# Kernel optimization log

Measured on AMD Instinct MI355X. Metric: run time of the kernel, lower is better.

The kernel has to match this reference:

```python
import jax, jax.numpy as jnp
import numpy as np

L, H, D, DFF, B, S = 4, 8, 512, 2048, 2, 2048
DH = D // H
EPS = 1e-5
SCALE_BASE = 512.0


def setup_inputs() -> dict:
    key = jax.random.key(0)
    ks = jax.random.split(key, 8)
    def w(k, shape, s=0.02):
        return jax.random.normal(k, shape, jnp.float32) * s
    return {
        "x": jax.random.normal(ks[0], (B, S, D), jnp.float32),
        "WQ": w(ks[1], (L, H, D, DH)),
        "WK": w(ks[2], (L, H, D, DH)),
        "WV": w(ks[3], (L, H, D, DH)),
        "WG": w(ks[4], (L, D, D)),
        "WO": w(ks[5], (L, D, D)),
        "gn_w": jnp.ones((L, D), jnp.float32),
        "gn_b": jnp.zeros((L, D), jnp.float32),
        "ln1_w": jnp.ones((L, D), jnp.float32),
        "ln1_b": jnp.zeros((L, D), jnp.float32),
        "ln2_w": jnp.ones((L, D), jnp.float32),
        "ln2_b": jnp.zeros((L, D), jnp.float32),
        "ffn_w1": w(ks[6], (L, D, DFF)),
        "ffn_b1": jnp.zeros((L, DFF), jnp.float32),
        "ffn_w2": w(ks[7], (L, DFF, D)),
        "ffn_b2": jnp.zeros((L, D), jnp.float32),
    }


def _dup(t):
    # duplicate_interleave: [a,b] -> [a,a,b,b]
    return jnp.repeat(t, 2, axis=-1)


def _rot(x):
    # rotate_every_two: (x1,x2) -> (-x2, x1)
    x1, x2 = x[..., ::2], x[..., 1::2]
    return jnp.stack([-x2, x1], axis=-1).reshape(x.shape)


def _xpos(x, downscale):
    # x: [B,H,S,dh]  XPOS rotary with length-extrapolating scale
    s_len, dh = x.shape[-2], x.shape[-1]
    half = dh // 2
    base = (jnp.arange(0, dh, 2, dtype=jnp.float32) + 0.4 * dh) / (1.4 * dh)  # [half]
    power = jnp.arange(s_len, dtype=jnp.float32) / SCALE_BASE
    scale = base[None, :] ** power[:, None]  # [S, half]
    if downscale:
        scale = 1.0 / scale
    inv_freq = 1.0 / (10000.0 ** (jnp.arange(half, dtype=jnp.float32) / half))
    ang = jnp.arange(s_len, dtype=jnp.float32)[:, None] * inv_freq[None, :]
    sin, cos, sc = _dup(jnp.sin(ang)), _dup(jnp.cos(ang)), _dup(scale)
    return x * cos * sc + _rot(x) * sin * sc


def _ln(x, w, b):
    mu = jnp.mean(x, -1, keepdims=True)
    var = jnp.mean((x - mu) ** 2, -1, keepdims=True)
    return (x - mu) * jax.lax.rsqrt(var + EPS) * w + b


def reference(x, WQ, WK, WV, WG, WO, gn_w, gn_b, ln1_w, ln1_b, ln2_w, ln2_b, ffn_w1, ffn_b1, ffn_w2, ffn_b2):
    gammas = 1.0 - jnp.exp(jnp.linspace(np.log(1.0 / 32.0), np.log(1.0 / 512.0), H)).astype(jnp.float32)
    idx = jnp.arange(S, dtype=jnp.float32)
    diff = idx[:, None] - idx[None, :]
    Dmask = jnp.where(diff >= 0, gammas[:, None, None] ** diff, 0.0)  # [H,S,S]
    b = x.shape[0]
    for i in range(L):
        xn = _ln(x, ln1_w[i], ln1_b[i])
        q = _xpos(jnp.einsum('bsd,hde->bhse', xn, WQ[i]), False)
        k = _xpos(jnp.einsum('bsd,hde->bhse', xn, WK[i]), True)
        v = jnp.einsum('bsd,hde->bhse', xn, WV[i])
        att = jnp.einsum('bhse,bhte->bhst', q, k) * Dmask[None]  # [B,H,S,S]
        yh = jnp.einsum('bhst,bhte->bhse', att, v)               # [B,H,S,dh]
        yh = yh.transpose(0, 2, 1, 3)                            # [B,S,H,dh]
        mu = jnp.mean(yh, -1, keepdims=True)
        var = jnp.mean((yh - mu) ** 2, -1, keepdims=True)
        yn = (yh - mu) * jax.lax.rsqrt(var + EPS)
        yn = yn * gn_w[i].reshape(H, DH) + gn_b[i].reshape(H, DH)
        y = yn.reshape(b, S, D)
        g = jax.nn.silu(xn @ WG[i])
        y1 = (g * y) @ WO[i] + x
        h = _ln(y1, ln2_w[i], ln2_b[i])
        x = jax.nn.gelu(h @ ffn_w1[i] + ffn_b1[i], approximate=False) @ ffn_w2[i] + ffn_b2[i] + y1
    return x
```

## Files before the change

### kernel.cpp

```cpp
#include <hip/hip_runtime.h>
#include <hip/hip_bf16.h>

#define LYR 4
#define NH  8
#define DM  512
#define DHD 64
#define DFF 2048
#define BB  2
#define SSL 2048
#define NROWS (BB*SSL)

typedef unsigned short u16;
typedef __attribute__((ext_vector_type(8))) short bf16x8;
typedef __attribute__((ext_vector_type(4))) float f32x4;
typedef __attribute__((ext_vector_type(4))) unsigned int u32x4;

__device__ __forceinline__ u16 f2bf(float f) {
    union { float f; unsigned u; } v; v.f = f;
    unsigned r = v.u + 0x7FFFu + ((v.u >> 16) & 1u);
    return (u16)(r >> 16);
}
__device__ __forceinline__ float bf2f(u16 b) {
    union { unsigned u; float f; } v; v.u = ((unsigned)b) << 16;
    return v.f;
}
__device__ __forceinline__ int swz(int row, int col) {
    return row * 64 + (col & 7) + ((((col >> 3) ^ row) & 7) << 3);
}
__device__ __forceinline__ int swzP(int row, int col) {
    return row * 128 + (col & 7) + ((((col >> 3) ^ row) & 15) << 3);
}
__device__ __forceinline__ void gload16(const u16* g, u16* l) {
    __builtin_amdgcn_global_load_lds(
        (const __attribute__((address_space(1))) unsigned int*)g,
        (__attribute__((address_space(3))) unsigned int*)l, 16, 0, 0);
}
template <int N> __device__ __forceinline__ void wait_vmcnt() {
    if constexpr (N == 0)      asm volatile("s_waitcnt vmcnt(0)" ::: "memory");
    else if constexpr (N == 6) asm volatile("s_waitcnt vmcnt(6)" ::: "memory");
    else if constexpr (N == 8) asm volatile("s_waitcnt vmcnt(8)" ::: "memory");
    else static_assert(N == 0 || N == 6 || N == 8, "unsupported vmcnt");
}
__device__ __forceinline__ void block_barrier() {
    __builtin_amdgcn_s_barrier();
    asm volatile("" ::: "memory");
}


__global__ __launch_bounds__(256) void xpos_tables(float4* __restrict__ tab4) {
    const int idx = blockIdx.x * 256 + threadIdx.x;
    const int s = idx >> 5, j = idx & 31;
    const float base = (2.f * j + 0.4f * 64.f) / (1.4f * 64.f);
    const float invf = powf(10000.f, -(float)j / 32.f);
    const float ang = (float)s * invf;
    const float scq = powf(base, (float)s / 512.f);
    tab4[idx] = make_float4(sinf(ang), cosf(ang), scq, 1.f / scq);
}

__global__ __launch_bounds__(256)
void prep_qkv(const float* __restrict__ WQp, const float* __restrict__ WKp,
              const float* __restrict__ WVp, u16* __restrict__ WBT) {
    const int dt = blockIdx.x;
    const int h = blockIdx.y & 7, which = blockIdx.y >> 3;
    const int l = blockIdx.z;
    const float* W = (which == 0 ? WQp : which == 1 ? WKp : WVp);
    const float* ip = W + ((size_t)(l * 8 + h)) * (512 * 64);
    u16* op = WBT + (size_t)l * (2048 * 512) + (size_t)(which * 512 + h * 64) * 512;
    __shared__ u16 tile[64 * 72];
    const int t = threadIdx.x, rr = t >> 2, cc = (t & 3) * 16;
    const float* src = ip + (size_t)(dt * 64 + rr) * 64 + cc;
#pragma unroll
    for (int i = 0; i < 16; ++i) tile[rr * 72 + cc + i] = f2bf(src[i]);
    __syncthreads();
    u16 tmp[16] __attribute__((aligned(16)));
#pragma unroll
    for (int i = 0; i < 16; ++i) tmp[i] = tile[(cc + i) * 72 + rr];
    u16* dst = op + (size_t)rr * 512 + dt * 64 + cc;
    *(u32x4*)&dst[0] = *(const u32x4*)&tmp[0];
    *(u32x4*)&dst[8] = *(const u32x4*)&tmp[8];
}

__global__ __launch_bounds__(256)
void prep_t(const float* __restrict__ in, u16* __restrict__ out, int R, int C,
            long long in_ls, long long out_ls) {
    const float* ip = in + (size_t)blockIdx.z * in_ls;
    u16* op = out + (size_t)blockIdx.z * out_ls;
    const int r0 = blockIdx.x * 64, c0t = blockIdx.y * 64;
    __shared__ u16 tile[64 * 72];
    const int t = threadIdx.x, rr = t >> 2, cc = (t & 3) * 16;
    const float* src = ip + (size_t)(r0 + rr) * C + c0t + cc;
#pragma unroll
    for (int i = 0; i < 16; ++i) tile[rr * 72 + cc + i] = f2bf(src[i]);
    __syncthreads();
    u16 tmp[16] __attribute__((aligned(16)));
#pragma unroll
    for (int i = 0; i < 16; ++i) tmp[i] = tile[(cc + i) * 72 + rr];
    u16* dst = op + (size_t)(c0t + rr) * R + r0 + cc;
    *(u32x4*)&dst[0] = *(const u32x4*)&tmp[0];
    *(u32x4*)&dst[8] = *(const u32x4*)&tmp[8];
}

__global__ __launch_bounds__(256)
void ln_kernel(const float* __restrict__ x, const float* __restrict__ wt,
               const float* __restrict__ bs, u16* __restrict__ out) {
    const int row = blockIdx.x * 4 + (threadIdx.x >> 6);
    const int lane = threadIdx.x & 63;
    const float* xr = x + (size_t)row * DM + lane * 8;
    float v[8];
    *(float4*)&v[0] = *(const float4*)&xr[0];
    *(float4*)&v[4] = *(const float4*)&xr[4];
    float s = 0.f, s2 = 0.f;
#pragma unroll
    for (int i = 0; i < 8; ++i) { s += v[i]; s2 += v[i] * v[i]; }
#pragma unroll
    for (int m = 1; m < 64; m <<= 1) {
        s  += __shfl_xor(s, m, 64);
        s2 += __shfl_xor(s2, m, 64);
    }
    const float mu = s * (1.f / DM);
    const float rs = rsqrtf(s2 * (1.f / DM) - mu * mu + 1e-5f);
    const int e0 = lane * 8;
    u16 o[8] __attribute__((aligned(16)));
#pragma unroll
    for (int i = 0; i < 8; ++i)
        o[i] = f2bf((v[i] - mu) * rs * wt[e0 + i] + bs[e0 + i]);
    *(u32x4*)&out[(size_t)row * DM + e0] = *(const u32x4*)o;
}

template <int BM, int BN, int EPI>
__global__ __launch_bounds__(256)
void gemm_bt(const u16* __restrict__ A, const u16* __restrict__ Bt,
             u16* __restrict__ obf, float* __restrict__ of32,
             const float* __restrict__ res, const float* __restrict__ bias,
             u16* __restrict__ qb, u16* __restrict__ kb, u16* __restrict__ vt,
             u16* __restrict__ gb, const float4* __restrict__ tab4,
             int M, int N, int K) {
    constexpr int FM = BM / 32, FN = BN / 32;
    constexpr int LPS = BM / 32 + BN / 32;
    static_assert(LPS == 6, "vmcnt template expects 6");
    __shared__ __align__(16) u16 As[2][BM * 64];
    __shared__ __align__(16) u16 Bs[2][BN * 64];
    const int t = threadIdx.x;
    const int lane = t & 63, w4 = t >> 6;
    const int wr = w4 >> 1, wc = w4 & 1;
    const int fr = lane & 15, fq = lane >> 4;
    const int nX = N / BN;
    const int nwg = (M / BM) * nX;
    const int swzid = (blockIdx.x & 7) * (nwg >> 3) + (blockIdx.x >> 3);
    const int m0 = (swzid / nX) * BM, n0 = (swzid % nX) * BN;
    const int lr = lane >> 3;
    const int ls = lane & 7;
    const int nsteps = K >> 6;

    auto stage = [&](int step, int slot) {
        const int k0 = step << 6;
#pragma unroll
        for (int q = 0; q < BM / 32; ++q) {
            const int ib = q * 4 + w4;
            const int row = ib * 8 + lr;
            const int cc = ls ^ (row & 7);
            gload16(&A[(size_t)(m0 + row) * K + k0 + cc * 8], &As[slot][ib * 512]);
        }
#pragma unroll
        for (int q = 0; q < BN / 32; ++q) {
            const int ib = q * 4 + w4;
            const int row = ib * 8 + lr;
            const int cc = ls ^ (row & 7);
            gload16(&Bt[(size_t)(n0 + row) * K + k0 + cc * 8], &Bs[slot][ib * 512]);
        }
    };

    f32x4 acc[FM][FN] = {};
    stage(0, 0);
    stage(1, 1);
    for (int st = 0; st < nsteps; ++st) {
        if (st + 1 < nsteps) wait_vmcnt<LPS>(); else wait_vmcnt<0>();
        __builtin_amdgcn_sched_barrier(0);
        block_barrier();
        const u16* Ac = As[st & 1];
        const u16* Bc = Bs[st & 1];
#pragma unroll
        for (int ks = 0; ks < 2; ++ks) {
            bf16x8 av[FM], bv[FN];
#pragma unroll
            for (int i = 0; i < FM; ++i)
                av[i] = *(const bf16x8*)&Ac[swz(wr * (BM / 2) + i * 16 + fr, ks * 32 + fq * 8)];
#pragma unroll
            for (int j = 0; j < FN; ++j)
                bv[j] = *(const bf16x8*)&Bc[swz(wc * (BN / 2) + j * 16 + fr, ks * 32 + fq * 8)];
#pragma unroll
            for (int i = 0; i < FM; ++i)
#pragma unroll
                for (int j = 0; j < FN; ++j)
                    acc[i][j] = __builtin_amdgcn_mfma_f32_16x16x32_bf16(av[i], bv[j], acc[i][j], 0, 0, 0);
        }
        asm volatile("s_waitcnt lgkmcnt(0)" ::: "memory");
        __builtin_amdgcn_sched_barrier(0);
        block_barrier();
        if (st + 2 < nsteps) stage(st + 2, st & 1);
    }

    if constexpr (EPI == 4) {
        const int region = n0 >> 9;
        const int h = (n0 & 511) >> 6;
        const int b = m0 >> 11;
        const int bh = b * NH + h;
        const int s0 = m0 & 2047;
        if (region == 3) {
#pragma unroll
            for (int i = 0; i < FM; ++i)
#pragma unroll
                for (int j = 0; j < FN; ++j)
#pragma unroll
                    for (int r = 0; r < 4; ++r) {
                        const int m = m0 + wr * (BM / 2) + i * 16 + fq * 4 + r;
                        const int e = wc * (BN / 2) + j * 16 + fr;
                        gb[(size_t)m * 512 + h * 64 + e] = f2bf(acc[i][j][r]);
                    }
        } else if (region <= 1) {
            u16* dst = (region == 0) ? qb : kb;
#pragma unroll
            for (int i = 0; i < FM; ++i)
#pragma unroll
                for (int j = 0; j < FN; ++j)
#pragma unroll
                    for (int r = 0; r < 4; ++r) {
                        const int s = s0 + wr * (BM / 2) + i * 16 + fq * 4 + r;
                        const int e = wc * (BN / 2) + j * 16 + fr;
                        const float v = acc[i][j][r];
                        const float p = __shfl_xor(v, 1, 64);
                        const float rot = (e & 1) ? p : -p;
                        const float4 t4 = tab4[(size_t)s * 32 + (e >> 1)];
                        const float scl = (region == 0) ? t4.z : t4.w;
                        dst[((size_t)bh * 2048 + s) * 64 + e] =
                            f2bf((v * t4.y + rot * t4.x) * scl);
                    }
        } else {
            constexpr int LTS = BM + 8;
            u16* LT = (u16*)As;
#pragma unroll
            for (int i = 0; i < FM; ++i)
#pragma unroll
                for (int j = 0; j < FN; ++j)
#pragma unroll
                    for (int r = 0; r < 4; ++r) {
                        const int sl = wr * (BM / 2) + i * 16 + fq * 4 + r;
                        const int e = wc * (BN / 2) + j * 16 + fr;
                        LT[e * LTS + sl] = f2bf(acc[i][j][r]);
                    }
            __syncthreads();
            for (int c = t; c < 64 * (BM / 8); c += 256) {
                const int er = c / (BM / 8);
                const int sc = (c % (BM / 8)) * 8;
                const u32x4 vrow = *(const u32x4*)&LT[er * LTS + sc];
                *(u32x4*)&vt[((size_t)bh * 64 + er) * 2048 + s0 + sc] = vrow;
            }
        }
    } else {
#pragma unroll
        for (int i = 0; i < FM; ++i)
#pragma unroll
            for (int j = 0; j < FN; ++j)
#pragma unroll
                for (int r = 0; r < 4; ++r) {
                    const int m = m0 + wr * (BM / 2) + i * 16 + fq * 4 + r;
                    const int n = n0 + wc * (BN / 2) + j * 16 + fr;
                    const size_t idx = (size_t)m * N + n;
                    float v = acc[i][j][r];
                    if constexpr (EPI == 0) {
                        obf[idx] = f2bf(v);
                    } else if constexpr (EPI == 1) {
                        of32[idx] = v + res[idx];
                    } else if constexpr (EPI == 2) {
                        float tt = v + bias[n];
                        obf[idx] = f2bf(0.5f * tt * (1.f + erff(tt * 0.7071067811865475f)));
                    } else {
                        of32[idx] = v + bias[n] + res[idx];
                    }
                }
    }
}

__global__ __launch_bounds__(512)
void retention(const u16* __restrict__ Qb, const u16* __restrict__ Kb,
               const u16* __restrict__ Vt, const u16* __restrict__ gate,
               const float* __restrict__ gnw, const float* __restrict__ gnb,
               u16* __restrict__ zb) {
    extern __shared__ __align__(16) char smem[];
    u16* KsB = (u16*)smem;
    u16* VsB = (u16*)(smem + 32768);
    u16* Qs  = (u16*)(smem + 65536);
    u16* Ps  = (u16*)(smem + 73728);

    const int logical = (blockIdx.x & 7) * 64 + (blockIdx.x >> 3);
    const int bh = logical >> 5;
    const int qt = 31 - (logical & 31);
    const int h = bh & 7, b = bh >> 3;
    const int t = threadIdx.x;
    const int lane = t & 63, w = t >> 6;
    const int fr = lane & 15, fq = lane >> 4;
    const int wr = w & 1, wc2 = w >> 1;
    const int oc = wc2 & 1, th = w >> 2;

    const float gamma = 1.f - expf(-3.4657359f + (float)h * -0.39608410f);
    const float lgam = log2f(gamma);
    const float dlim = 19.931568f / (-lgam);
    const int jt_last = (qt * 64 + 63) >> 7;
    int jt_min = 0;
    {
        const float need = (float)(qt * 64 - 127) - dlim;
        if (need > 0.f) jt_min = (int)ceilf(need * (1.f / 128.f));
        if (jt_min > jt_last) jt_min = jt_last;
        if (jt_min < 0) jt_min = 0;
    }

    float rowf[2][4], colf[2];
#pragma unroll
    for (int i = 0; i < 2; ++i)
#pragma unroll
        for (int rr = 0; rr < 4; ++rr)
            rowf[i][rr] = exp2f((float)(wr * 32 + i * 16 + fq * 4 + rr) * lgam);
#pragma unroll
    for (int j = 0; j < 2; ++j)
        colf[j] = exp2f(-(float)(wc2 * 32 + j * 16 + fr) * lgam);

    const size_t bh2048 = (size_t)bh * 2048;
    const int lr8 = lane >> 3, ls8 = lane & 7;
    const int lr16 = lane >> 4, ls16 = lane & 15;

    {
        const int row = w * 8 + lr8;
        const int cc = ls8 ^ (row & 7);
        gload16(&Qb[(bh2048 + qt * 64 + row) * 64 + cc * 8], &Qs[w * 512]);
    }

    f32x4 oacc[2][2] = {};
    int cur = 0;
    {
        const int jt = jt_min;
        u16* Kd = KsB; u16* Vd = VsB;
#pragma unroll
        for (int q = 0; q < 2; ++q) {
            const int row = q * 64 + w * 8 + lr8;
            const int cc = ls8 ^ (row & 7);
            gload16(&Kb[(bh2048 + jt * 128 + row) * 64 + cc * 8], &Kd[(q * 64 + w * 8) * 64]);
        }
#pragma unroll
        for (int q = 0; q < 2; ++q) {
            const int row = w * 8 + q * 4 + lr16;
            const int cc = ls16 ^ (row & 15);
            gload16(&Vt[((size_t)bh * 64 + row) * 2048 + jt * 128 + cc * 8], &Vd[(w * 8 + q * 4) * 128]);
        }
    }

    for (int jt = jt_min; jt <= jt_last; ++jt) {
        __syncthreads();
        if (jt < jt_last) {
            const int nb = cur ^ 1;
            u16* Kd = KsB + nb * 8192;
            u16* Vd = VsB + nb * 8192;
#pragma unroll
            for (int q = 0; q < 2; ++q) {
                const int row = q * 64 + w * 8 + lr8;
                const int cc = ls8 ^ (row & 7);
                gload16(&Kb[(bh2048 + (jt + 1) * 128 + row) * 64 + cc * 8], &Kd[(q * 64 + w * 8) * 64]);
            }
#pragma unroll
            for (int q = 0; q < 2; ++q) {
                const int row = w * 8 + q * 4 + lr16;
                const int cc = ls16 ^ (row & 15);
                gload16(&Vt[((size_t)bh * 64 + row) * 2048 + (jt + 1) * 128 + cc * 8], &Vd[(w * 8 + q * 4) * 128]);
            }
        }
        const u16* Kc = KsB + cur * 8192;
        f32x4 sac[2][2] = {};
#pragma unroll
        for (int ks = 0; ks < 2; ++ks) {
            bf16x8 qa[2], kb2[2];
#pragma unroll
            for (int i = 0; i < 2; ++i)
                qa[i] = *(const bf16x8*)&Qs[swz(wr * 32 + i * 16 + fr, ks * 32 + fq * 8)];
#pragma unroll
            for (int j = 0; j < 2; ++j)
                kb2[j] = *(const bf16x8*)&Kc[swz(wc2 * 32 + j * 16 + fr, ks * 32 + fq * 8)];
#pragma unroll
            for (int i = 0; i < 2; ++i)
#pragma unroll
                for (int j = 0; j < 2; ++j)
                    sac[i][j] = __builtin_amdgcn_mfma_f32_16x16x32_bf16(qa[i], kb2[j], sac[i][j], 0, 0, 0);
        }
        const float sc = exp2f((float)(qt * 64 - jt * 128) * lgam);
        const bool diag = (jt == jt_last);
#pragma unroll
        for (int i = 0; i < 2; ++i)
#pragma unroll
            for (int j = 0; j < 2; ++j)
#pragma unroll
                for (int rr = 0; rr < 4; ++rr) {
                    float m = sc * rowf[i][rr] * colf[j];
                    if (diag) {
                        const int d = (qt * 64 + wr * 32 + i * 16 + fq * 4 + rr)
                                    - (jt * 128 + wc2 * 32 + j * 16 + fr);
                        if (d < 0) m = 0.f;
                    }
                    Ps[swzP(wr * 32 + i * 16 + fq * 4 + rr, wc2 * 32 + j * 16 + fr)] =
                        f2bf(sac[i][j][rr] * m);
                }
        __syncthreads();
        const u16* Vc = VsB + cur * 8192;
#pragma unroll
        for (int ks = 0; ks < 2; ++ks) {
            const int tcol = th * 64 + ks * 32 + fq * 8;
            bf16x8 pa[2], vb[2];
#pragma unroll
            for (int i = 0; i < 2; ++i)
                pa[i] = *(const bf16x8*)&Ps[swzP(wr * 32 + i * 16 + fr, tcol)];
#pragma unroll
            for (int j = 0; j < 2; ++j)
                vb[j] = *(const bf16x8*)&Vc[swzP(oc * 32 + j * 16 + fr, tcol)];
#pragma unroll
            for (int i = 0; i < 2; ++i)
#pragma unroll
                for (int j = 0; j < 2; ++j)
                    oacc[i][j] = __builtin_amdgcn_mfma_f32_16x16x32_bf16(pa[i], vb[j], oacc[i][j], 0, 0, 0);
        }
        cur ^= 1;
    }

    __syncthreads();
    float* Of = (float*)smem;
    if (th == 1) {
#pragma unroll
        for (int i = 0; i < 2; ++i)
#pragma unroll
            for (int j = 0; j < 2; ++j)
#pragma unroll
                for (int rr = 0; rr < 4; ++rr)
                    Of[(wr * 32 + i * 16 + fq * 4 + rr) * 66 + oc * 32 + j * 16 + fr] = oacc[i][j][rr];
    }
    __syncthreads();
    if (th == 0) {
#pragma unroll
        for (int i = 0; i < 2; ++i)
#pragma unroll
            for (int j = 0; j < 2; ++j)
#pragma unroll
                for (int rr = 0; rr < 4; ++rr) {
                    const int idx = (wr * 32 + i * 16 + fq * 4 + rr) * 66 + oc * 32 + j * 16 + fr;
                    Of[idx] += oacc[i][j][rr];
                }
    }
    __syncthreads();
    const int row = t >> 3, c0 = (t & 7) * 8;
    float v[8];
    float s = 0.f, s2 = 0.f;
#pragma unroll
    for (int i = 0; i < 8; ++i) {
        v[i] = Of[row * 66 + c0 + i];
        s += v[i]; s2 += v[i] * v[i];
    }
    s  += __shfl_xor(s, 1, 64);  s  += __shfl_xor(s, 2, 64);  s  += __shfl_xor(s, 4, 64);
    s2 += __shfl_xor(s2, 1, 64); s2 += __shfl_xor(s2, 2, 64); s2 += __shfl_xor(s2, 4, 64);
    const float mu = s * (1.f / 64.f);
    const float rs = rsqrtf(s2 * (1.f / 64.f) - mu * mu + 1e-5f);
    const int sg = qt * 64 + row;
    u16 gv[8] __attribute__((aligned(16)));
    *(u32x4*)gv = *(const u32x4*)&gate[((size_t)(b * SSL + sg)) * 512 + h * 64 + c0];
    u16 ob[8] __attribute__((aligned(16)));
#pragma unroll
    for (int i = 0; i < 8; ++i) {
        const int dc = h * 64 + c0 + i;
        const float yn = (v[i] - mu) * rs * gnw[dc] + gnb[dc];
        const float g = bf2f(gv[i]);
        ob[i] = f2bf(yn * (g / (1.f + expf(-g))));
    }
    *(u32x4*)&zb[((size_t)(b * SSL + sg)) * 512 + h * 64 + c0] = *(const u32x4*)ob;
}

extern "C" void kernel_launch(void* const* d_in, const int* in_sizes, int n_in,
                              void* d_out, int out_size, void* d_ws, size_t ws_size,
                              hipStream_t stream) {
    const float* X    = (const float*)d_in[0];
    const float* WQ   = (const float*)d_in[1];
    const float* WK   = (const float*)d_in[2];
    const float* WV   = (const float*)d_in[3];
    const float* WG   = (const float*)d_in[4];
    const float* WO   = (const float*)d_in[5];
    const float* GNW  = (const float*)d_in[6];
    const float* GNB  = (const float*)d_in[7];
    const float* LN1W = (const float*)d_in[8];
    const float* LN1B = (const float*)d_in[9];
    const float* LN2W = (const float*)d_in[10];
    const float* LN2B = (const float*)d_in[11];
    const float* FW1  = (const float*)d_in[12];
    const float* FB1  = (const float*)d_in[13];
    const float* FW2  = (const float*)d_in[14];
    const float* FB2  = (const float*)d_in[15];

    char* ws = (char*)d_ws;
    size_t off = 0;
    auto alloc = [&](size_t n) { char* p = ws + off; off += (n + 255) & ~(size_t)255; return p; };

    u16*   WBT  = (u16*)alloc((size_t)LYR * 2048 * 512 * 2);
    u16*   WOT  = (u16*)alloc((size_t)LYR * 512 * 512 * 2);
    u16*   W1T  = (u16*)alloc((size_t)LYR * 2048 * 512 * 2);
    u16*   W2T  = (u16*)alloc((size_t)LYR * 512 * 2048 * 2);
    float4* TAB4 = (float4*)alloc((size_t)2048 * 32 * 16);
    float* XB   = (float*)alloc((size_t)NROWS * DM * 4);
    u16*   XN   = (u16*)alloc((size_t)NROWS * DM * 2);
    u16*   FF1  = (u16*)alloc((size_t)NROWS * 2048 * 2);
    u16*   GB   = (u16*)alloc((size_t)NROWS * DM * 2);
    u16*   QBp  = (u16*)alloc((size_t)NROWS * DM * 2);
    u16*   KBp  = (u16*)alloc((size_t)NROWS * DM * 2);
    u16*   VTp  = (u16*)alloc((size_t)NROWS * DM * 2);
    u16*   ZB   = (u16*)alloc((size_t)NROWS * DM * 2);
    float* Y1   = (float*)alloc((size_t)NROWS * DM * 4);
    u16*   HB   = QBp;

    xpos_tables<<<256, 256, 0, stream>>>(TAB4);
    prep_qkv<<<dim3(8, 24, LYR), 256, 0, stream>>>(WQ, WK, WV, WBT);
    prep_t<<<dim3(8, 8, LYR), 256, 0, stream>>>(WG, WBT + 1536 * 512, 512, 512,
                                                (long long)512 * 512, (long long)2048 * 512);
    prep_t<<<dim3(8, 8, LYR), 256, 0, stream>>>(WO, WOT, 512, 512,
                                                (long long)512 * 512, (long long)512 * 512);
    prep_t<<<dim3(8, 32, LYR), 256, 0, stream>>>(FW1, W1T, 512, 2048,
                                                 (long long)512 * 2048, (long long)2048 * 512);
    prep_t<<<dim3(32, 8, LYR), 256, 0, stream>>>(FW2, W2T, 2048, 512,
                                                 (long long)2048 * 512, (long long)512 * 2048);

    for (int l = 0; l < LYR; ++l) {
        const float* xsrc = (l == 0) ? X : XB;
        float* xdst = (l == LYR - 1) ? (float*)d_out : XB;
        ln_kernel<<<NROWS / 4, 256, 0, stream>>>(xsrc, LN1W + l * 512, LN1B + l * 512, XN);
        gemm_bt<128, 64, 4><<<1024, 256, 0, stream>>>(
            XN, WBT + (size_t)l * 2048 * 512, nullptr, nullptr, nullptr, nullptr,
            QBp, KBp, VTp, GB, TAB4, NROWS, 2048, 512);
        retention<<<512, 512, 90112, stream>>>(QBp, KBp, VTp, GB,
                                               GNW + l * 512, GNB + l * 512, ZB);
        gemm_bt<64, 128, 1><<<256, 256, 0, stream>>>(
            ZB, WOT + (size_t)l * 512 * 512, nullptr, Y1, xsrc, nullptr,
            nullptr, nullptr, nullptr, nullptr, nullptr, NROWS, 512, 512);
        ln_kernel<<<NROWS / 4, 256, 0, stream>>>(Y1, LN2W + l * 512, LN2B + l * 512, HB);
        gemm_bt<128, 64, 2><<<1024, 256, 0, stream>>>(
            HB, W1T + (size_t)l * 2048 * 512, FF1, nullptr, nullptr, FB1 + l * 2048,
            nullptr, nullptr, nullptr, nullptr, nullptr, NROWS, 2048, 512);
        gemm_bt<64, 128, 3><<<256, 256, 0, stream>>>(
            FF1, W2T + (size_t)l * 512 * 2048, nullptr, xdst, Y1, FB2 + l * 512,
            nullptr, nullptr, nullptr, nullptr, nullptr, NROWS, 512, 2048);
    }
}
```

Before: 477.3 us.

## Add 256x128 tiled 512-thread GEMM for QKV/gate and FFN1 projections

Adds a new gemm_big kernel with 256x128 tiles, 8 waves per block and launch_bounds(512,1). It replaces the 128x64 gemm_bt for the QKV+gate projection and the FFN up-projection with GELU. The larger tiles raise operand reuse from LDS and cut the block count from 1024 to 256, and s_setprio is raised around the MFMA loop. The XPOS and V-transpose epilogues are adapted so one tile can span two heads. In exchange there are fewer blocks to spread across CUs (256) and more register pressure from 16 accumulators per wave.

```diff
diff --git a/kernel.cpp b/kernel.cpp
--- a/kernel.cpp
+++ b/kernel.cpp
@@ -38,8 +38,7 @@
 template <int N> __device__ __forceinline__ void wait_vmcnt() {
     if constexpr (N == 0)      asm volatile("s_waitcnt vmcnt(0)" ::: "memory");
     else if constexpr (N == 6) asm volatile("s_waitcnt vmcnt(6)" ::: "memory");
-    else if constexpr (N == 8) asm volatile("s_waitcnt vmcnt(8)" ::: "memory");
-    else static_assert(N == 0 || N == 6 || N == 8, "unsupported vmcnt");
+    else static_assert(N == 0 || N == 6, "unsupported vmcnt");
 }
 __device__ __forceinline__ void block_barrier() {
     __builtin_amdgcn_s_barrier();
@@ -132,8 +131,6 @@
 void gemm_bt(const u16* __restrict__ A, const u16* __restrict__ Bt,
              u16* __restrict__ obf, float* __restrict__ of32,
              const float* __restrict__ res, const float* __restrict__ bias,
-             u16* __restrict__ qb, u16* __restrict__ kb, u16* __restrict__ vt,
-             u16* __restrict__ gb, const float4* __restrict__ tab4,
              int M, int N, int K) {
     constexpr int FM = BM / 32, FN = BN / 32;
     constexpr int LPS = BM / 32 + BN / 32;
@@ -199,85 +196,161 @@
         block_barrier();
         if (st + 2 < nsteps) stage(st + 2, st & 1);
     }
-
-    if constexpr (EPI == 4) {
+#pragma unroll
+    for (int i = 0; i < FM; ++i)
+#pragma unroll
+        for (int j = 0; j < FN; ++j)
+#pragma unroll
+            for (int r = 0; r < 4; ++r) {
+                const int m = m0 + wr * (BM / 2) + i * 16 + fq * 4 + r;
+                const int n = n0 + wc * (BN / 2) + j * 16 + fr;
+                const size_t idx = (size_t)m * N + n;
+                float v = acc[i][j][r];
+                if constexpr (EPI == 1) {
+                    of32[idx] = v + res[idx];
+                } else {
+                    of32[idx] = v + bias[n] + res[idx];
+                }
+            }
+}
+
+template <int EPI>
+__global__ __launch_bounds__(512, 1)
+void gemm_big(const u16* __restrict__ A, const u16* __restrict__ Bt,
+              u16* __restrict__ obf, const float* __restrict__ bias,
+              u16* __restrict__ qb, u16* __restrict__ kb, u16* __restrict__ vt,
+              u16* __restrict__ gb, const float4* __restrict__ tab4,
+              int M, int N, int K) {
+    constexpr int BM = 256, BN = 128;
+    __shared__ __align__(16) u16 SM[49152];
+    const int t = threadIdx.x;
+    const int lane = t & 63, w = t >> 6;
+    const int wr = w >> 2, wcn = w & 3;
+    const int fr = lane & 15, fq = lane >> 4;
+    const int nX = N / BN;
+    const int nwg = (M / BM) * nX;
+    const int swzid = (blockIdx.x & 7) * (nwg >> 3) + (blockIdx.x >> 3);
+    const int m0 = (swzid / nX) * BM, n0 = (swzid % nX) * BN;
+    const int lr = lane >> 3, ls = lane & 7;
+    const int nsteps = K >> 6;
+
+    auto stage = [&](int step, int slot) {
+        const int k0 = step << 6;
+#pragma unroll
+        for (int q = 0; q < 4; ++q) {
+            const int ib = q * 8 + w;
+            const int row = ib * 8 + lr;
+            const int cc = ls ^ (row & 7);
+            gload16(&A[(size_t)(m0 + row) * K + k0 + cc * 8], &SM[slot * 16384 + ib * 512]);
+        }
+#pragma unroll
+        for (int q = 0; q < 2; ++q) {
+            const int ib = q * 8 + w;
+            const int row = ib * 8 + lr;
+            const int cc = ls ^ (row & 7);
+            gload16(&Bt[(size_t)(n0 + row) * K + k0 + cc * 8],
+                    &SM[32768 + slot * 8192 + ib * 512]);
+        }
+    };
+
+    f32x4 acc[8][2] = {};
+    stage(0, 0);
+    stage(1, 1);
+    for (int st = 0; st < nsteps; ++st) {
+        if (st + 1 < nsteps) wait_vmcnt<6>(); else wait_vmcnt<0>();
+        __builtin_amdgcn_sched_barrier(0);
+        block_barrier();
+        const u16* Ac = &SM[(st & 1) * 16384];
+        const u16* Bc = &SM[32768 + (st & 1) * 8192];
+#pragma unroll
+        for (int ks = 0; ks < 2; ++ks) {
+            bf16x8 bv[2];
+#pragma unroll
+            for (int j = 0; j < 2; ++j)
+                bv[j] = *(const bf16x8*)&Bc[swz(wcn * 32 + j * 16 + fr, ks * 32 + fq * 8)];
+            __builtin_amdgcn_s_setprio(1);
+#pragma unroll
+            for (int i = 0; i < 8; ++i) {
+                bf16x8 av = *(const bf16x8*)&Ac[swz(wr * 128 + i * 16 + fr, ks * 32 + fq * 8)];
+                acc[i][0] = __builtin_amdgcn_mfma_f32_16x16x32_bf16(av, bv[0], acc[i][0], 0, 0, 0);
+                acc[i][1] = __builtin_amdgcn_mfma_f32_16x16x32_bf16(av, bv[1], acc[i][1], 0, 0, 0);
+            }
+            __builtin_amdgcn_s_setprio(0);
+        }
+        asm volatile("s_waitcnt lgkmcnt(0)" ::: "memory");
+        __builtin_amdgcn_sched_barrier(0);
+        block_barrier();
+        if (st + 2 < nsteps) stage(st + 2, st & 1);
+    }
+
+    if constexpr (EPI == 2) {
+#pragma unroll
+        for (int i = 0; i < 8; ++i)
+#pragma unroll
+            for (int j = 0; j < 2; ++j)
+#pragma unroll
+                for (int r = 0; r < 4; ++r) {
+                    const int m = m0 + wr * 128 + i * 16 + fq * 4 + r;
+                    const int n = n0 + wcn * 32 + j * 16 + fr;
+                    float tt = acc[i][j][r] + bias[n];
+                    obf[(size_t)m * N + n] = f2bf(0.5f * tt * (1.f + erff(tt * 0.7071067811865475f)));
+                }
+    } else {
         const int region = n0 >> 9;
         const int h = (n0 & 511) >> 6;
         const int b = m0 >> 11;
-        const int bh = b * NH + h;
         const int s0 = m0 & 2047;
         if (region == 3) {
 #pragma unroll
-            for (int i = 0; i < FM; ++i)
-#pragma unroll
-                for (int j = 0; j < FN; ++j)
+            for (int i = 0; i < 8; ++i)
+#pragma unroll
+                for (int j = 0; j < 2; ++j)
 #pragma unroll
                     for (int r = 0; r < 4; ++r) {
-                        const int m = m0 + wr * (BM / 2) + i * 16 + fq * 4 + r;
-                        const int e = wc * (BN / 2) + j * 16 + fr;
-                        gb[(size_t)m * 512 + h * 64 + e] = f2bf(acc[i][j][r]);
+                        const int m = m0 + wr * 128 + i * 16 + fq * 4 + r;
+                        const int el = wcn * 32 + j * 16 + fr;
+                        gb[(size_t)m * 512 + (n0 & 511) + el] = f2bf(acc[i][j][r]);
                     }
         } else if (region <= 1) {
             u16* dst = (region == 0) ? qb : kb;
 #pragma unroll
-            for (int i = 0; i < FM; ++i)
-#pragma unroll
-                for (int j = 0; j < FN; ++j)
+            for (int i = 0; i < 8; ++i)
+#pragma unroll
+                for (int j = 0; j < 2; ++j)
 #pragma unroll
                     for (int r = 0; r < 4; ++r) {
-                        const int s = s0 + wr * (BM / 2) + i * 16 + fq * 4 + r;
-                        const int e = wc * (BN / 2) + j * 16 + fr;
+                        const int s = s0 + wr * 128 + i * 16 + fq * 4 + r;
+                        const int el = wcn * 32 + j * 16 + fr;
+                        const int hh = h + (el >> 6), e = el & 63;
                         const float v = acc[i][j][r];
                         const float p = __shfl_xor(v, 1, 64);
                         const float rot = (e & 1) ? p : -p;
                         const float4 t4 = tab4[(size_t)s * 32 + (e >> 1)];
                         const float scl = (region == 0) ? t4.z : t4.w;
-                        dst[((size_t)bh * 2048 + s) * 64 + e] =
+                        dst[((size_t)(b * NH + hh) * 2048 + s) * 64 + e] =
                             f2bf((v * t4.y + rot * t4.x) * scl);
                     }
         } else {
-            constexpr int LTS = BM + 8;
-            u16* LT = (u16*)As;
-#pragma unroll
-            for (int i = 0; i < FM; ++i)
-#pragma unroll
-                for (int j = 0; j < FN; ++j)
+            u16* LT = SM;
+#pragma unroll
+            for (int i = 0; i < 8; ++i)
+#pragma unroll
+                for (int j = 0; j < 2; ++j)
 #pragma unroll
                     for (int r = 0; r < 4; ++r) {
-                        const int sl = wr * (BM / 2) + i * 16 + fq * 4 + r;
-                        const int e = wc * (BN / 2) + j * 16 + fr;
-                        LT[e * LTS + sl] = f2bf(acc[i][j][r]);
+                        const int sl = wr * 128 + i * 16 + fq * 4 + r;
+                        const int el = wcn * 32 + j * 16 + fr;
+                        LT[el * 264 + sl] = f2bf(acc[i][j][r]);
                     }
             __syncthreads();
-            for (int c = t; c < 64 * (BM / 8); c += 256) {
-                const int er = c / (BM / 8);
-                const int sc = (c % (BM / 8)) * 8;
-                const u32x4 vrow = *(const u32x4*)&LT[er * LTS + sc];
-                *(u32x4*)&vt[((size_t)bh * 64 + er) * 2048 + s0 + sc] = vrow;
+            for (int c = t; c < 128 * 32; c += 512) {
+                const int er = c >> 5;
+                const int sc = (c & 31) * 8;
+                const int hh = h + (er >> 6), e = er & 63;
+                *(u32x4*)&vt[((size_t)(b * NH + hh) * 64 + e) * 2048 + s0 + sc] =
+                    *(const u32x4*)&LT[er * 264 + sc];
             }
         }
-    } else {
-#pragma unroll
-        for (int i = 0; i < FM; ++i)
-#pragma unroll
-            for (int j = 0; j < FN; ++j)
-#pragma unroll
-                for (int r = 0; r < 4; ++r) {
-                    const int m = m0 + wr * (BM / 2) + i * 16 + fq * 4 + r;
-                    const int n = n0 + wc * (BN / 2) + j * 16 + fr;
-                    const size_t idx = (size_t)m * N + n;
-                    float v = acc[i][j][r];
-                    if constexpr (EPI == 0) {
-                        obf[idx] = f2bf(v);
-                    } else if constexpr (EPI == 1) {
-                        of32[idx] = v + res[idx];
-                    } else if constexpr (EPI == 2) {
-                        float tt = v + bias[n];
-                        obf[idx] = f2bf(0.5f * tt * (1.f + erff(tt * 0.7071067811865475f)));
-                    } else {
-                        of32[idx] = v + bias[n] + res[idx];
-                    }
-                }
     }
 }
 
@@ -532,20 +605,18 @@
         const float* xsrc = (l == 0) ? X : XB;
         float* xdst = (l == LYR - 1) ? (float*)d_out : XB;
         ln_kernel<<<NROWS / 4, 256, 0, stream>>>(xsrc, LN1W + l * 512, LN1B + l * 512, XN);
-        gemm_bt<128, 64, 4><<<1024, 256, 0, stream>>>(
-            XN, WBT + (size_t)l * 2048 * 512, nullptr, nullptr, nullptr, nullptr,
+        gemm_big<4><<<256, 512, 0, stream>>>(
+            XN, WBT + (size_t)l * 2048 * 512, nullptr, nullptr,
             QBp, KBp, VTp, GB, TAB4, NROWS, 2048, 512);
         retention<<<512, 512, 90112, stream>>>(QBp, KBp, VTp, GB,
                                                GNW + l * 512, GNB + l * 512, ZB);
         gemm_bt<64, 128, 1><<<256, 256, 0, stream>>>(
-            ZB, WOT + (size_t)l * 512 * 512, nullptr, Y1, xsrc, nullptr,
-            nullptr, nullptr, nullptr, nullptr, nullptr, NROWS, 512, 512);
+            ZB, WOT + (size_t)l * 512 * 512, nullptr, Y1, xsrc, nullptr, NROWS, 512, 512);
         ln_kernel<<<NROWS / 4, 256, 0, stream>>>(Y1, LN2W + l * 512, LN2B + l * 512, HB);
-        gemm_bt<128, 64, 2><<<1024, 256, 0, stream>>>(
-            HB, W1T + (size_t)l * 2048 * 512, FF1, nullptr, nullptr, FB1 + l * 2048,
+        gemm_big<2><<<256, 512, 0, stream>>>(
+            HB, W1T + (size_t)l * 2048 * 512, FF1, FB1 + l * 2048,
             nullptr, nullptr, nullptr, nullptr, nullptr, NROWS, 2048, 512);
         gemm_bt<64, 128, 3><<<256, 256, 0, stream>>>(
-            FF1, W2T + (size_t)l * 512 * 2048, nullptr, xdst, Y1, FB2 + l * 512,
-            nullptr, nullptr, nullptr, nullptr, nullptr, NROWS, 512, 2048);
-    }
-}
+            FF1, W2T + (size_t)l * 512 * 2048, nullptr, xdst, Y1, FB2 + l * 512, NROWS, 512, 2048);
+    }
+}
```

New measurement: 455.9 us (median of 2 runs). -4.5%, faster.
